# Kernel optimization log

Hardware: AMD Instinct MI355X
Metric: run time of the kernel (lower is better)

## Reference

```python
import jax, jax.numpy as jnp
import numpy as np

B, T, D, UNITS, NUM_OUT = 64, 1024, 256, 256, 32


def setup_inputs() -> dict:
    key = jax.random.key(0)
    k1, k2, k3 = jax.random.split(key, 3)
    inputs = jax.random.normal(k1, (B, T, D), dtype=jnp.float32)
    U = jax.random.normal(k2, (D, 4 * UNITS), dtype=jnp.float32) * 0.05
    W = jax.random.normal(k3, (UNITS, 4 * UNITS), dtype=jnp.float32) * 0.05
    b = jnp.zeros((4 * UNITS,), dtype=jnp.float32)
    return {"inputs": inputs, "U": U, "W": W, "b": b, "num_outputs": NUM_OUT}


def reference(inputs, U, W, b, num_outputs):
    # inputs: [B, T, D]; U: [D, 4u]; W: [u, 4u]; b: [4u]
    Bsz, Tlen, _ = inputs.shape
    units = W.shape[0]
    # Precompute input projection as one batched GEMM (x_t @ U + b for all t)
    xz = jnp.einsum('btd,dk->btk', inputs, U) + b  # [B, T, 4u]

    def step(carry, xz_t):
        h, c = carry
        z = xz_t + h @ W  # [B, 4u]
        z0, z1, z2, z3 = jnp.split(z, 4, axis=1)
        i = jax.nn.sigmoid(z0)
        f = jax.nn.sigmoid(z1)
        c_new = f * c + i * jnp.tanh(z2)
        o = jax.nn.sigmoid(z3)
        h_new = o * jnp.tanh(c_new)
        return (h_new, c_new), h_new

    h0 = jnp.zeros((Bsz, units), dtype=inputs.dtype)
    c0 = jnp.zeros((Bsz, units), dtype=inputs.dtype)
    (_, _), hs = jax.lax.scan(step, (h0, c0), jnp.swapaxes(xz, 0, 1))  # hs: [T, B, u]
    outputs = jnp.swapaxes(hs, 0, 1)[:, Tlen - num_outputs:, :]  # [B, num_outputs, u]
    return outputs
```

## Files before the change

### kernel.cpp

```cpp
#include <hip/hip_runtime.h>
#include <hip/hip_fp16.h>
#include <stdint.h>

#define Bsz 64
#define Tsz 1024
#define Dsz 256
#define UNITSn 256
#define Zdim 1024

typedef _Float16 half2v __attribute__((ext_vector_type(2)));
typedef _Float16 f16x8  __attribute__((ext_vector_type(8)));
typedef float    f32x4  __attribute__((ext_vector_type(4)));

__device__ __forceinline__ float dot2acc(uint32_t w, uint32_t h, float acc) {
#if __has_builtin(__builtin_amdgcn_fdot2)
  return __builtin_amdgcn_fdot2(__builtin_bit_cast(half2v, w),
                                __builtin_bit_cast(half2v, h), acc, false);
#else
  __half2 wv = __builtin_bit_cast(__half2, w);
  __half2 hv = __builtin_bit_cast(__half2, h);
  acc = fmaf(__half2float(__low2half(wv)),  __half2float(__low2half(hv)),  acc);
  acc = fmaf(__half2float(__high2half(wv)), __half2float(__high2half(hv)), acc);
  return acc;
#endif
}

__device__ __forceinline__ float dot4(const uint4& w, const uint4& h, float acc) {
  acc = dot2acc(w.x, h.x, acc); acc = dot2acc(w.y, h.y, acc);
  acc = dot2acc(w.z, h.z, acc); acc = dot2acc(w.w, h.w, acc);
  return acc;
}

__device__ __forceinline__ float sigm(float x)   { return 1.0f / (1.0f + __expf(-x)); }
__device__ __forceinline__ float tanh_f(float x) { return 1.0f - 2.0f / (__expf(2.0f * x) + 1.0f); }

__global__ __launch_bounds__(256) void convert_u(const float* __restrict__ U,
                                                 _Float16* __restrict__ UT) {
  int i = blockIdx.x * 256 + threadIdx.x;
  int n = i >> 8, k = i & 255;
  UT[i] = (_Float16)U[(size_t)k * Zdim + n];
}

__global__ __launch_bounds__(256) void convert_w5(const float* __restrict__ W,
                                                  uint4* __restrict__ Wop,
                                                  uint4* __restrict__ Wlds,
                                                  uint4* __restrict__ Wstr) {
  int i = blockIdx.x * 256 + threadIdx.x;
  if (i >= 32768) return;
  int t, g, k2base, outIdx;
  uint4* dst;
  if (i < 8192) {
    int j = i >> 9; t = i & 511; g = j & 3; k2base = (j >> 2) * 4;
    dst = Wop; outIdx = i;
  } else if (i < 14336) {
    int i2 = i - 8192; int cl = i2 >> 9; t = i2 & 511; g = cl & 3;
    k2base = 16 + (cl >> 2) * 4; dst = Wlds; outIdx = i2;
  } else {
    int i3 = i - 14336; int kb = i3 >> 11; int r = i3 & 2047;
    t = r >> 2; g = r & 3; k2base = 28 + kb * 4; dst = Wstr; outIdx = i3;
  }
  int col = g * 256 + (t & 255);
  int kbase = (t >> 8) * 64 + k2base;
  uint32_t d[4];
#pragma unroll
  for (int e = 0; e < 4; e++) {
    int k2 = kbase + e;
    float w0 = W[(size_t)(2 * k2) * Zdim + col];
    float w1 = W[(size_t)(2 * k2 + 1) * Zdim + col];
    __half2 p = __floats2half2_rn(w0, w1);
    d[e] = __builtin_bit_cast(uint32_t, p);
  }
  dst[outIdx] = make_uint4(d[0], d[1], d[2], d[3]);
}

__global__ __launch_bounds__(256) void proj_mfma(
    const float* __restrict__ x, const _Float16* __restrict__ UT,
    const float* __restrict__ bias, float* __restrict__ xz, int t0) {
  __shared__ _Float16 Ax[64][40];
  __shared__ _Float16 Ux[256][40];
  const int tid  = threadIdx.x;
  const int w    = tid >> 6, lane = tid & 63;
  const int lr   = lane & 15, kg = lane >> 4;
  const int n0   = blockIdx.x * 256;
  const int tloc = blockIdx.y;
  const int t    = t0 + tloc;
  const int arow = tid >> 2, ak = (tid & 3) * 8;

  f32x4 acc[4][4];
#pragma unroll
  for (int mi = 0; mi < 4; mi++)
#pragma unroll
    for (int ni = 0; ni < 4; ni++) acc[mi][ni] = f32x4{0.f, 0.f, 0.f, 0.f};

  for (int k0 = 0; k0 < Dsz; k0 += 32) {
    const float* xp = x + ((size_t)arow * Tsz + t) * Dsz + k0 + ak;
    float4 p0 = *(const float4*)xp;
    float4 p1 = *(const float4*)(xp + 4);
    const _Float16* up = UT + (size_t)(n0 + tid) * Dsz + k0;
    f16x8 u0 = *(const f16x8*)up;
    f16x8 u1 = *(const f16x8*)(up + 8);
    f16x8 u2 = *(const f16x8*)(up + 16);
    f16x8 u3 = *(const f16x8*)(up + 24);
    __syncthreads();
    f16x8 a8;
    a8[0] = (_Float16)p0.x; a8[1] = (_Float16)p0.y;
    a8[2] = (_Float16)p0.z; a8[3] = (_Float16)p0.w;
    a8[4] = (_Float16)p1.x; a8[5] = (_Float16)p1.y;
    a8[6] = (_Float16)p1.z; a8[7] = (_Float16)p1.w;
    *(f16x8*)&Ax[arow][ak] = a8;
    *(f16x8*)&Ux[tid][0]  = u0;
    *(f16x8*)&Ux[tid][8]  = u1;
    *(f16x8*)&Ux[tid][16] = u2;
    *(f16x8*)&Ux[tid][24] = u3;
    __syncthreads();
    f16x8 af[4], uf[4];
#pragma unroll
    for (int mi = 0; mi < 4; mi++) af[mi] = *(const f16x8*)&Ax[mi * 16 + lr][kg * 8];
#pragma unroll
    for (int ni = 0; ni < 4; ni++) uf[ni] = *(const f16x8*)&Ux[w * 64 + ni * 16 + lr][kg * 8];
#pragma unroll
    for (int mi = 0; mi < 4; mi++)
#pragma unroll
      for (int ni = 0; ni < 4; ni++)
        acc[mi][ni] = __builtin_amdgcn_mfma_f32_16x16x32_f16(af[mi], uf[ni],
                                                             acc[mi][ni], 0, 0, 0);
  }
#pragma unroll
  for (int ni = 0; ni < 4; ni++) {
    int col = n0 + w * 64 + ni * 16 + lr;
    float bs = bias[col];
#pragma unroll
    for (int mi = 0; mi < 4; mi++) {
      f32x4 v = acc[mi][ni];
#pragma unroll
      for (int r = 0; r < 4; r++) {
        int brow = mi * 16 + kg * 4 + r;
        xz[((size_t)tloc * 64 + brow) * Zdim + col] = v[r] + bs;
      }
    }
  }
}

__global__ __launch_bounds__(512) void lstm_chunk(
    const float* __restrict__ xz, const uint4* __restrict__ Wop,
    const uint4* __restrict__ WldsBuf, const uint4* __restrict__ Wstr,
    float* __restrict__ out, uint4* __restrict__ h_state,
    float* __restrict__ c_state, int t0, int Tc, int n_out) {
  extern __shared__ uint4 smem4[];
  uint4*  Wl = smem4;
  uint4*  hq = smem4 + 6144;
  float4* pp = (float4*)(smem4 + 6144 + 64);

  const int tid  = threadIdx.x;
  const int b    = blockIdx.x;
  const int half = tid >> 8, u = tid & 255;

  uint4 wop[16];
#pragma unroll
  for (int j = 0; j < 16; j++) wop[j] = Wop[(size_t)j * 512 + tid];
#pragma unroll
  for (int j = 0; j < 16; j++)
    asm volatile("" : "+v"(wop[j].x), "+v"(wop[j].y), "+v"(wop[j].z), "+v"(wop[j].w));
#pragma unroll
  for (int cl = 0; cl < 12; cl++)
    Wl[(size_t)cl * 512 + tid] = WldsBuf[(size_t)cl * 512 + tid];

  float c = 0.0f;
  if (t0 == 0) {
    if (tid < 64) hq[tid] = make_uint4(0, 0, 0, 0);
  } else {
    if (tid < 32) hq[tid] = h_state[(size_t)b * 32 + tid];
    if (half == 0) c = c_state[(size_t)b * 256 + u];
  }
  __syncthreads();

  const float* xzb = xz + (size_t)b * Zdim + u;
  float nx0 = 0, nx1 = 0, nx2 = 0, nx3 = 0;
  if (half == 0) { nx0 = xzb[0]; nx1 = xzb[256]; nx2 = xzb[512]; nx3 = xzb[768]; }
  const uint4* wstr = Wstr + (size_t)tid * 4;

#define LDB(s, kb) { const uint4* p_ = wstr + (size_t)(kb) * 2048; \
    s[0] = p_[0]; s[1] = p_[1]; s[2] = p_[2]; s[3] = p_[3]; }
#define USEB(s, hi) { uint4 h4_ = hb[hi]; \
    a0 = dot4(s[0], h4_, a0); a1 = dot4(s[1], h4_, a1); \
    a2 = dot4(s[2], h4_, a2); a3 = dot4(s[3], h4_, a3); }
#define LDSPH(jj2) { uint4 h4_ = hb[4 + (jj2)]; \
    uint4 w0_ = Wl[(size_t)((jj2) * 4 + 0) * 512 + tid]; \
    uint4 w1_ = Wl[(size_t)((jj2) * 4 + 1) * 512 + tid]; \
    uint4 w2_ = Wl[(size_t)((jj2) * 4 + 2) * 512 + tid]; \
    uint4 w3_ = Wl[(size_t)((jj2) * 4 + 3) * 512 + tid]; \
    a0 = dot4(w0_, h4_, a0); a1 = dot4(w1_, h4_, a1); \
    a2 = dot4(w2_, h4_, a2); a3 = dot4(w3_, h4_, a3); }

  for (int tl = 0; tl < Tc; tl++) {
    const int buf = tl & 1;
    const uint4* hb = hq + buf * 32 + half * 16;
    float a0 = 0, a1 = 0, a2 = 0, a3 = 0;
    uint4 sA[4], sB[4];
    LDB(sA, 0); LDB(sB, 1);
#pragma unroll
    for (int jj = 0; jj < 4; jj++) {
      uint4 h4 = hb[jj];
      a0 = dot4(wop[jj * 4 + 0], h4, a0);
      a1 = dot4(wop[jj * 4 + 1], h4, a1);
      a2 = dot4(wop[jj * 4 + 2], h4, a2);
      a3 = dot4(wop[jj * 4 + 3], h4, a3);
    }
    USEB(sA, 7);  LDB(sA, 2);
    LDSPH(0);
    USEB(sB, 8);  LDB(sB, 3);
    LDSPH(1);
    USEB(sA, 9);  LDB(sA, 4);
    LDSPH(2);
    USEB(sB, 10); LDB(sB, 5);
    USEB(sA, 11); LDB(sA, 6);
    USEB(sB, 12); LDB(sB, 7);
    USEB(sA, 13); LDB(sA, 8);
    USEB(sB, 14);
    USEB(sA, 15);

    if (half) pp[u] = make_float4(a0, a1, a2, a3);
    __syncthreads();
    if (!half) {
      float4 q = pp[u];
      float z0 = a0 + q.x + nx0, z1 = a1 + q.y + nx1;
      float z2 = a2 + q.z + nx2, z3 = a3 + q.w + nx3;
      if (tl + 1 < Tc) {
        const float* xn = xzb + (size_t)(tl + 1) * (Bsz * Zdim);
        nx0 = xn[0]; nx1 = xn[256]; nx2 = xn[512]; nx3 = xn[768];
      }
      float ig = sigm(z0), fg = sigm(z1), gg = tanh_f(z2), og = sigm(z3);
      c = fg * c + ig * gg;
      float hn = og * tanh_f(c);
      int ot = (t0 + tl) - (Tsz - n_out);
      if (ot >= 0) out[((size_t)b * n_out + ot) * UNITSn + u] = hn;
      ((__half*)(hq + (buf ^ 1) * 32))[u] = __float2half(hn);
    }
    __syncthreads();
  }
  if (tid < 32) h_state[(size_t)b * 32 + tid] = hq[(Tc & 1) * 32 + tid];
  if (half == 0) c_state[(size_t)b * 256 + u] = c;
#undef LDB
#undef USEB
#undef LDSPH
}

extern "C" void kernel_launch(void* const* d_in, const int* in_sizes, int n_in,
                              void* d_out, int out_size, void* d_ws, size_t ws_size,
                              hipStream_t stream) {
  const float* x    = (const float*)d_in[0];
  const float* U    = (const float*)d_in[1];
  const float* W    = (const float*)d_in[2];
  const float* bias = (const float*)d_in[3];
  float* out = (float*)d_out;
  const int n_out = out_size / (Bsz * UNITSn);

  uint8_t* ws = (uint8_t*)d_ws;
  uint4* Wop      = (uint4*)ws;
  uint4* Wlds     = (uint4*)(ws + (128u << 10));
  uint4* Wstr     = (uint4*)(ws + (224u << 10));
  _Float16* UT    = (_Float16*)(ws + (512u << 10));
  uint4* h_state  = (uint4*)(ws + (1024u << 10));
  float* c_state  = (float*)(ws + (1056u << 10));
  float* xz       = (float*)(ws + (2u << 20));

  int Tc = Tsz;
  while (Tc > 1 && (size_t)(2u << 20) + (size_t)Tc * (Bsz * Zdim) * 4 > ws_size) Tc >>= 1;

  convert_w5<<<dim3(128), dim3(256), 0, stream>>>(W, Wop, Wlds, Wstr);
  convert_u<<<dim3(1024), dim3(256), 0, stream>>>(U, UT);

  const int ldsBytes = (6144 + 64 + 256) * 16;
  hipFuncSetAttribute((const void*)lstm_chunk,
                      hipFuncAttributeMaxDynamicSharedMemorySize, ldsBytes);

  for (int t0 = 0; t0 < Tsz; t0 += Tc) {
    proj_mfma<<<dim3(4, Tc), dim3(256), 0, stream>>>(x, UT, bias, xz, t0);
    lstm_chunk<<<dim3(Bsz), dim3(512), ldsBytes, stream>>>(xz, Wop, Wlds, Wstr,
                                                           out, h_state, c_state,
                                                           t0, Tc, n_out);
  }
}
```

Before: 1.813 ms.

## Split recurrent K-dimension across four thread quarters per batch block

The recurrent LSTM kernel moves from 512 threads (two K-halves) to 1024 threads (four K-quarters) per batch row, so each thread handles 64 of the 256 hidden inputs. The weight split changes to match: 16 register slots, 8 LDS slots and 8 streamed-from-global slots per thread, with the converter rewritten for the new layout. Partial sums from three quarters go through LDS and quarter 0 reduces them, aiming to shorten the serial per-timestep dot-product chain. The dot product now uses inline v_dot2_f32_f16 asm instead of the builtin. In exchange it uses more LDS, more threads and a larger reduction per step.

```diff
diff --git a/kernel.cpp b/kernel.cpp
--- a/kernel.cpp
+++ b/kernel.cpp
@@ -8,21 +8,12 @@
 #define UNITSn 256
 #define Zdim 1024
 
-typedef _Float16 half2v __attribute__((ext_vector_type(2)));
 typedef _Float16 f16x8  __attribute__((ext_vector_type(8)));
 typedef float    f32x4  __attribute__((ext_vector_type(4)));
 
 __device__ __forceinline__ float dot2acc(uint32_t w, uint32_t h, float acc) {
-#if __has_builtin(__builtin_amdgcn_fdot2)
-  return __builtin_amdgcn_fdot2(__builtin_bit_cast(half2v, w),
-                                __builtin_bit_cast(half2v, h), acc, false);
-#else
-  __half2 wv = __builtin_bit_cast(__half2, w);
-  __half2 hv = __builtin_bit_cast(__half2, h);
-  acc = fmaf(__half2float(__low2half(wv)),  __half2float(__low2half(hv)),  acc);
-  acc = fmaf(__half2float(__high2half(wv)), __half2float(__high2half(hv)), acc);
+  asm("v_dot2_f32_f16 %0, %1, %2, %0" : "+v"(acc) : "v"(w), "v"(h));
   return acc;
-#endif
 }
 
 __device__ __forceinline__ float dot4(const uint4& w, const uint4& h, float acc) {
@@ -41,26 +32,21 @@
   UT[i] = (_Float16)U[(size_t)k * Zdim + n];
 }
 
-__global__ __launch_bounds__(256) void convert_w5(const float* __restrict__ W,
+__global__ __launch_bounds__(256) void convert_w6(const float* __restrict__ W,
                                                   uint4* __restrict__ Wop,
                                                   uint4* __restrict__ Wlds,
                                                   uint4* __restrict__ Wstr) {
   int i = blockIdx.x * 256 + threadIdx.x;
   if (i >= 32768) return;
-  int t, g, k2base, outIdx;
+  int slot = i >> 10, t = i & 1023;
+  int q = t >> 8, u = t & 255;
+  int g, j, outIdx;
   uint4* dst;
-  if (i < 8192) {
-    int j = i >> 9; t = i & 511; g = j & 3; k2base = (j >> 2) * 4;
-    dst = Wop; outIdx = i;
-  } else if (i < 14336) {
-    int i2 = i - 8192; int cl = i2 >> 9; t = i2 & 511; g = cl & 3;
-    k2base = 16 + (cl >> 2) * 4; dst = Wlds; outIdx = i2;
-  } else {
-    int i3 = i - 14336; int kb = i3 >> 11; int r = i3 & 2047;
-    t = r >> 2; g = r & 3; k2base = 28 + kb * 4; dst = Wstr; outIdx = i3;
-  }
-  int col = g * 256 + (t & 255);
-  int kbase = (t >> 8) * 64 + k2base;
+  if (slot < 16)      { g = slot >> 2;      j = slot & 3;            dst = Wop;  outIdx = slot * 1024 + t; }
+  else if (slot < 24) { int cl = slot - 16; g = cl & 3; j = 4 + (cl >> 2); dst = Wlds; outIdx = cl * 1024 + t; }
+  else                { int ss = slot - 24; g = ss & 3; j = 6 + (ss >> 2); dst = Wstr; outIdx = ss * 1024 + t; }
+  int col = g * 256 + u;
+  int kbase = q * 32 + j * 4;
   uint32_t d[4];
 #pragma unroll
   for (int e = 0; e < 4; e++) {
@@ -141,90 +127,85 @@
   }
 }
 
-__global__ __launch_bounds__(512) void lstm_chunk(
-    const float* __restrict__ xz, const uint4* __restrict__ Wop,
-    const uint4* __restrict__ WldsBuf, const uint4* __restrict__ Wstr,
-    float* __restrict__ out, uint4* __restrict__ h_state,
-    float* __restrict__ c_state, int t0, int Tc, int n_out) {
+__global__ __launch_bounds__(1024)
+__attribute__((amdgpu_waves_per_eu(4, 4)))
+void lstm_chunk(const float* __restrict__ xz, const uint4* __restrict__ Wop,
+                const uint4* __restrict__ WldsBuf, const uint4* __restrict__ Wstr,
+                float* __restrict__ out, uint4* __restrict__ h_state,
+                float* __restrict__ c_state, int t0, int Tc, int n_out) {
   extern __shared__ uint4 smem4[];
   uint4*  Wl = smem4;
-  uint4*  hq = smem4 + 6144;
-  float4* pp = (float4*)(smem4 + 6144 + 64);
-
-  const int tid  = threadIdx.x;
-  const int b    = blockIdx.x;
-  const int half = tid >> 8, u = tid & 255;
+  uint4*  hq = smem4 + 8192;
+  float4* pp = (float4*)(smem4 + 8192 + 64);
+
+  const int tid = threadIdx.x;
+  const int b   = blockIdx.x;
+  const int q   = tid >> 8, u = tid & 255;
 
   uint4 wop[16];
 #pragma unroll
-  for (int j = 0; j < 16; j++) wop[j] = Wop[(size_t)j * 512 + tid];
+  for (int j = 0; j < 16; j++) wop[j] = Wop[(size_t)j * 1024 + tid];
 #pragma unroll
   for (int j = 0; j < 16; j++)
     asm volatile("" : "+v"(wop[j].x), "+v"(wop[j].y), "+v"(wop[j].z), "+v"(wop[j].w));
 #pragma unroll
-  for (int cl = 0; cl < 12; cl++)
-    Wl[(size_t)cl * 512 + tid] = WldsBuf[(size_t)cl * 512 + tid];
+  for (int cl = 0; cl < 8; cl++)
+    Wl[(size_t)cl * 1024 + tid] = WldsBuf[(size_t)cl * 1024 + tid];
 
   float c = 0.0f;
   if (t0 == 0) {
     if (tid < 64) hq[tid] = make_uint4(0, 0, 0, 0);
   } else {
     if (tid < 32) hq[tid] = h_state[(size_t)b * 32 + tid];
-    if (half == 0) c = c_state[(size_t)b * 256 + u];
+    if (q == 0)   c = c_state[(size_t)b * 256 + u];
   }
   __syncthreads();
 
   const float* xzb = xz + (size_t)b * Zdim + u;
   float nx0 = 0, nx1 = 0, nx2 = 0, nx3 = 0;
-  if (half == 0) { nx0 = xzb[0]; nx1 = xzb[256]; nx2 = xzb[512]; nx3 = xzb[768]; }
-  const uint4* wstr = Wstr + (size_t)tid * 4;
-
-#define LDB(s, kb) { const uint4* p_ = wstr + (size_t)(kb) * 2048; \
-    s[0] = p_[0]; s[1] = p_[1]; s[2] = p_[2]; s[3] = p_[3]; }
-#define USEB(s, hi) { uint4 h4_ = hb[hi]; \
-    a0 = dot4(s[0], h4_, a0); a1 = dot4(s[1], h4_, a1); \
-    a2 = dot4(s[2], h4_, a2); a3 = dot4(s[3], h4_, a3); }
-#define LDSPH(jj2) { uint4 h4_ = hb[4 + (jj2)]; \
-    uint4 w0_ = Wl[(size_t)((jj2) * 4 + 0) * 512 + tid]; \
-    uint4 w1_ = Wl[(size_t)((jj2) * 4 + 1) * 512 + tid]; \
-    uint4 w2_ = Wl[(size_t)((jj2) * 4 + 2) * 512 + tid]; \
-    uint4 w3_ = Wl[(size_t)((jj2) * 4 + 3) * 512 + tid]; \
-    a0 = dot4(w0_, h4_, a0); a1 = dot4(w1_, h4_, a1); \
-    a2 = dot4(w2_, h4_, a2); a3 = dot4(w3_, h4_, a3); }
+  if (q == 0) { nx0 = xzb[0]; nx1 = xzb[256]; nx2 = xzb[512]; nx3 = xzb[768]; }
+  const uint4* wstr = Wstr + tid;
 
   for (int tl = 0; tl < Tc; tl++) {
     const int buf = tl & 1;
-    const uint4* hb = hq + buf * 32 + half * 16;
+    const uint4* hb = hq + buf * 32 + q * 8;
     float a0 = 0, a1 = 0, a2 = 0, a3 = 0;
-    uint4 sA[4], sB[4];
-    LDB(sA, 0); LDB(sB, 1);
-#pragma unroll
-    for (int jj = 0; jj < 4; jj++) {
-      uint4 h4 = hb[jj];
-      a0 = dot4(wop[jj * 4 + 0], h4, a0);
-      a1 = dot4(wop[jj * 4 + 1], h4, a1);
-      a2 = dot4(wop[jj * 4 + 2], h4, a2);
-      a3 = dot4(wop[jj * 4 + 3], h4, a3);
-    }
-    USEB(sA, 7);  LDB(sA, 2);
-    LDSPH(0);
-    USEB(sB, 8);  LDB(sB, 3);
-    LDSPH(1);
-    USEB(sA, 9);  LDB(sA, 4);
-    LDSPH(2);
-    USEB(sB, 10); LDB(sB, 5);
-    USEB(sA, 11); LDB(sA, 6);
-    USEB(sB, 12); LDB(sB, 7);
-    USEB(sA, 13); LDB(sA, 8);
-    USEB(sB, 14);
-    USEB(sA, 15);
-
-    if (half) pp[u] = make_float4(a0, a1, a2, a3);
-    __syncthreads();
-    if (!half) {
-      float4 q = pp[u];
-      float z0 = a0 + q.x + nx0, z1 = a1 + q.y + nx1;
-      float z2 = a2 + q.z + nx2, z3 = a3 + q.w + nx3;
+
+    uint4 sA0 = wstr[0], sA1 = wstr[1024], sA2 = wstr[2048], sA3 = wstr[3072];
+#pragma unroll
+    for (int j = 0; j < 4; j++) {
+      uint4 h4 = hb[j];
+      a0 = dot4(wop[0 * 4 + j], h4, a0);
+      a1 = dot4(wop[1 * 4 + j], h4, a1);
+      a2 = dot4(wop[2 * 4 + j], h4, a2);
+      a3 = dot4(wop[3 * 4 + j], h4, a3);
+    }
+    uint4 sB0 = wstr[4096], sB1 = wstr[5120], sB2 = wstr[6144], sB3 = wstr[7168];
+#pragma unroll
+    for (int jj = 0; jj < 2; jj++) {
+      uint4 h4 = hb[4 + jj];
+      uint4 w0 = Wl[(size_t)(jj * 4 + 0) * 1024 + tid];
+      uint4 w1 = Wl[(size_t)(jj * 4 + 1) * 1024 + tid];
+      uint4 w2 = Wl[(size_t)(jj * 4 + 2) * 1024 + tid];
+      uint4 w3 = Wl[(size_t)(jj * 4 + 3) * 1024 + tid];
+      a0 = dot4(w0, h4, a0); a1 = dot4(w1, h4, a1);
+      a2 = dot4(w2, h4, a2); a3 = dot4(w3, h4, a3);
+    }
+    { uint4 h4 = hb[6];
+      a0 = dot4(sA0, h4, a0); a1 = dot4(sA1, h4, a1);
+      a2 = dot4(sA2, h4, a2); a3 = dot4(sA3, h4, a3); }
+    { uint4 h4 = hb[7];
+      a0 = dot4(sB0, h4, a0); a1 = dot4(sB1, h4, a1);
+      a2 = dot4(sB2, h4, a2); a3 = dot4(sB3, h4, a3); }
+
+    if (q) pp[(size_t)(q - 1) * 256 + u] = make_float4(a0, a1, a2, a3);
+    __syncthreads();
+    if (!q) {
+      float4 p0 = pp[u], p1 = pp[256 + u], p2 = pp[512 + u];
+      float z0 = a0 + p0.x + p1.x + p2.x + nx0;
+      float z1 = a1 + p0.y + p1.y + p2.y + nx1;
+      float z2 = a2 + p0.z + p1.z + p2.z + nx2;
+      float z3 = a3 + p0.w + p1.w + p2.w + nx3;
       if (tl + 1 < Tc) {
         const float* xn = xzb + (size_t)(tl + 1) * (Bsz * Zdim);
         nx0 = xn[0]; nx1 = xn[256]; nx2 = xn[512]; nx3 = xn[768];
@@ -239,10 +220,7 @@
     __syncthreads();
   }
   if (tid < 32) h_state[(size_t)b * 32 + tid] = hq[(Tc & 1) * 32 + tid];
-  if (half == 0) c_state[(size_t)b * 256 + u] = c;
-#undef LDB
-#undef USEB
-#undef LDSPH
+  if (q == 0)   c_state[(size_t)b * 256 + u] = c;
 }
 
 extern "C" void kernel_launch(void* const* d_in, const int* in_sizes, int n_in,
@@ -257,8 +235,8 @@
 
   uint8_t* ws = (uint8_t*)d_ws;
   uint4* Wop      = (uint4*)ws;
-  uint4* Wlds     = (uint4*)(ws + (128u << 10));
-  uint4* Wstr     = (uint4*)(ws + (224u << 10));
+  uint4* Wlds     = (uint4*)(ws + (256u << 10));
+  uint4* Wstr     = (uint4*)(ws + (384u << 10));
   _Float16* UT    = (_Float16*)(ws + (512u << 10));
   uint4* h_state  = (uint4*)(ws + (1024u << 10));
   float* c_state  = (float*)(ws + (1056u << 10));
@@ -267,17 +245,17 @@
   int Tc = Tsz;
   while (Tc > 1 && (size_t)(2u << 20) + (size_t)Tc * (Bsz * Zdim) * 4 > ws_size) Tc >>= 1;
 
-  convert_w5<<<dim3(128), dim3(256), 0, stream>>>(W, Wop, Wlds, Wstr);
+  convert_w6<<<dim3(128), dim3(256), 0, stream>>>(W, Wop, Wlds, Wstr);
   convert_u<<<dim3(1024), dim3(256), 0, stream>>>(U, UT);
 
-  const int ldsBytes = (6144 + 64 + 256) * 16;
+  const int ldsBytes = (8192 + 64 + 768) * 16;
   hipFuncSetAttribute((const void*)lstm_chunk,
                       hipFuncAttributeMaxDynamicSharedMemorySize, ldsBytes);
 
   for (int t0 = 0; t0 < Tsz; t0 += Tc) {
     proj_mfma<<<dim3(4, Tc), dim3(256), 0, stream>>>(x, UT, bias, xz, t0);
-    lstm_chunk<<<dim3(Bsz), dim3(512), ldsBytes, stream>>>(xz, Wop, Wlds, Wstr,
-                                                           out, h_state, c_state,
-                                                           t0, Tc, n_out);
-  }
-}
+    lstm_chunk<<<dim3(Bsz), dim3(1024), ldsBytes, stream>>>(xz, Wop, Wlds, Wstr,
+                                                            out, h_state, c_state,
+                                                            t0, Tc, n_out);
+  }
+}
```

New measurement: 2.241 ms. +23.7%, slower.

## Hold more recurrent weights in registers and cut streamed global loads in LSTM step

Applied to the files above, without the earlier changes.

The split of the recurrent weight matrix W across storage tiers changes: registers now hold 40 uint4 slices per thread (up from 16), LDS keeps 12, and the part streamed from global/L2 each timestep shrinks from 9 blocks of 4 to 3 blocks of 4. The conversion kernel is rewritten to match the new layout, shared memory becomes static, and the dot product uses inline v_dot2_f32_f16 asm. The aim is to cut per-step global memory traffic on the serial recurrence critical path. The cost is much higher VGPR pressure (160 registers just for weights), which risks spills or an occupancy limit at 512 threads.

```diff
diff --git a/kernel.cpp b/kernel.cpp
--- a/kernel.cpp
+++ b/kernel.cpp
@@ -8,21 +8,12 @@
 #define UNITSn 256
 #define Zdim 1024
 
-typedef _Float16 half2v __attribute__((ext_vector_type(2)));
 typedef _Float16 f16x8  __attribute__((ext_vector_type(8)));
 typedef float    f32x4  __attribute__((ext_vector_type(4)));
 
 __device__ __forceinline__ float dot2acc(uint32_t w, uint32_t h, float acc) {
-#if __has_builtin(__builtin_amdgcn_fdot2)
-  return __builtin_amdgcn_fdot2(__builtin_bit_cast(half2v, w),
-                                __builtin_bit_cast(half2v, h), acc, false);
-#else
-  __half2 wv = __builtin_bit_cast(__half2, w);
-  __half2 hv = __builtin_bit_cast(__half2, h);
-  acc = fmaf(__half2float(__low2half(wv)),  __half2float(__low2half(hv)),  acc);
-  acc = fmaf(__half2float(__high2half(wv)), __half2float(__high2half(hv)), acc);
+  asm("v_dot2_f32_f16 %0, %1, %2, %0" : "+v"(acc) : "v"(w), "v"(h));
   return acc;
-#endif
 }
 
 __device__ __forceinline__ float dot4(const uint4& w, const uint4& h, float acc) {
@@ -41,26 +32,20 @@
   UT[i] = (_Float16)U[(size_t)k * Zdim + n];
 }
 
-__global__ __launch_bounds__(256) void convert_w5(const float* __restrict__ W,
+__global__ __launch_bounds__(256) void convert_w7(const float* __restrict__ W,
                                                   uint4* __restrict__ Wop,
                                                   uint4* __restrict__ Wlds,
                                                   uint4* __restrict__ Wstr) {
   int i = blockIdx.x * 256 + threadIdx.x;
   if (i >= 32768) return;
-  int t, g, k2base, outIdx;
+  int slot = i >> 9, t = i & 511;
+  int g, jx, outIdx;
   uint4* dst;
-  if (i < 8192) {
-    int j = i >> 9; t = i & 511; g = j & 3; k2base = (j >> 2) * 4;
-    dst = Wop; outIdx = i;
-  } else if (i < 14336) {
-    int i2 = i - 8192; int cl = i2 >> 9; t = i2 & 511; g = cl & 3;
-    k2base = 16 + (cl >> 2) * 4; dst = Wlds; outIdx = i2;
-  } else {
-    int i3 = i - 14336; int kb = i3 >> 11; int r = i3 & 2047;
-    t = r >> 2; g = r & 3; k2base = 28 + kb * 4; dst = Wstr; outIdx = i3;
-  }
+  if (slot < 40)      { g = slot / 10;      jx = slot % 10;        dst = Wop;  outIdx = slot * 512 + t; }
+  else if (slot < 52) { int ss = slot - 40; g = ss & 3; jx = 10 + (ss >> 2); dst = Wlds; outIdx = ss * 512 + t; }
+  else                { int ss = slot - 52; g = ss & 3; jx = 13 + (ss >> 2); dst = Wstr; outIdx = ss * 512 + t; }
   int col = g * 256 + (t & 255);
-  int kbase = (t >> 8) * 64 + k2base;
+  int kbase = (t >> 8) * 64 + jx * 4;
   uint32_t d[4];
 #pragma unroll
   for (int e = 0; e < 4; e++) {
@@ -146,20 +131,19 @@
     const uint4* __restrict__ WldsBuf, const uint4* __restrict__ Wstr,
     float* __restrict__ out, uint4* __restrict__ h_state,
     float* __restrict__ c_state, int t0, int Tc, int n_out) {
-  extern __shared__ uint4 smem4[];
-  uint4*  Wl = smem4;
-  uint4*  hq = smem4 + 6144;
-  float4* pp = (float4*)(smem4 + 6144 + 64);
+  __shared__ uint4 Wl[12 * 512];
+  __shared__ uint4 hq[2][32];
+  __shared__ float4 pp[256];
 
   const int tid  = threadIdx.x;
   const int b    = blockIdx.x;
   const int half = tid >> 8, u = tid & 255;
 
-  uint4 wop[16];
-#pragma unroll
-  for (int j = 0; j < 16; j++) wop[j] = Wop[(size_t)j * 512 + tid];
-#pragma unroll
-  for (int j = 0; j < 16; j++)
+  uint4 wop[40];
+#pragma unroll
+  for (int j = 0; j < 40; j++) wop[j] = Wop[(size_t)j * 512 + tid];
+#pragma unroll
+  for (int j = 0; j < 40; j++)
     asm volatile("" : "+v"(wop[j].x), "+v"(wop[j].y), "+v"(wop[j].z), "+v"(wop[j].w));
 #pragma unroll
   for (int cl = 0; cl < 12; cl++)
@@ -167,9 +151,9 @@
 
   float c = 0.0f;
   if (t0 == 0) {
-    if (tid < 64) hq[tid] = make_uint4(0, 0, 0, 0);
+    if (tid < 64) ((uint4*)hq)[tid] = make_uint4(0, 0, 0, 0);
   } else {
-    if (tid < 32) hq[tid] = h_state[(size_t)b * 32 + tid];
+    if (tid < 32) ((uint4*)hq)[tid] = h_state[(size_t)b * 32 + tid];
     if (half == 0) c = c_state[(size_t)b * 256 + u];
   }
   __syncthreads();
@@ -177,47 +161,50 @@
   const float* xzb = xz + (size_t)b * Zdim + u;
   float nx0 = 0, nx1 = 0, nx2 = 0, nx3 = 0;
   if (half == 0) { nx0 = xzb[0]; nx1 = xzb[256]; nx2 = xzb[512]; nx3 = xzb[768]; }
-  const uint4* wstr = Wstr + (size_t)tid * 4;
-
-#define LDB(s, kb) { const uint4* p_ = wstr + (size_t)(kb) * 2048; \
-    s[0] = p_[0]; s[1] = p_[1]; s[2] = p_[2]; s[3] = p_[3]; }
-#define USEB(s, hi) { uint4 h4_ = hb[hi]; \
-    a0 = dot4(s[0], h4_, a0); a1 = dot4(s[1], h4_, a1); \
-    a2 = dot4(s[2], h4_, a2); a3 = dot4(s[3], h4_, a3); }
-#define LDSPH(jj2) { uint4 h4_ = hb[4 + (jj2)]; \
-    uint4 w0_ = Wl[(size_t)((jj2) * 4 + 0) * 512 + tid]; \
-    uint4 w1_ = Wl[(size_t)((jj2) * 4 + 1) * 512 + tid]; \
-    uint4 w2_ = Wl[(size_t)((jj2) * 4 + 2) * 512 + tid]; \
-    uint4 w3_ = Wl[(size_t)((jj2) * 4 + 3) * 512 + tid]; \
-    a0 = dot4(w0_, h4_, a0); a1 = dot4(w1_, h4_, a1); \
-    a2 = dot4(w2_, h4_, a2); a3 = dot4(w3_, h4_, a3); }
+  const uint4* wstr = Wstr + tid;
 
   for (int tl = 0; tl < Tc; tl++) {
     const int buf = tl & 1;
-    const uint4* hb = hq + buf * 32 + half * 16;
+    const uint4* hb = hq[buf] + half * 16;
     float a0 = 0, a1 = 0, a2 = 0, a3 = 0;
-    uint4 sA[4], sB[4];
-    LDB(sA, 0); LDB(sB, 1);
-#pragma unroll
-    for (int jj = 0; jj < 4; jj++) {
-      uint4 h4 = hb[jj];
-      a0 = dot4(wop[jj * 4 + 0], h4, a0);
-      a1 = dot4(wop[jj * 4 + 1], h4, a1);
-      a2 = dot4(wop[jj * 4 + 2], h4, a2);
-      a3 = dot4(wop[jj * 4 + 3], h4, a3);
+
+    uint4 s00 = wstr[0 * 512], s01 = wstr[1 * 512], s02 = wstr[2 * 512], s03 = wstr[3 * 512];
+    uint4 s10 = wstr[4 * 512], s11 = wstr[5 * 512], s12 = wstr[6 * 512], s13 = wstr[7 * 512];
+
+#pragma unroll
+    for (int j = 0; j < 10; j++) {
+      uint4 h4 = hb[j];
+      a0 = dot4(wop[0 * 10 + j], h4, a0);
+      a1 = dot4(wop[1 * 10 + j], h4, a1);
+      a2 = dot4(wop[2 * 10 + j], h4, a2);
+      a3 = dot4(wop[3 * 10 + j], h4, a3);
     }
-    USEB(sA, 7);  LDB(sA, 2);
-    LDSPH(0);
-    USEB(sB, 8);  LDB(sB, 3);
-    LDSPH(1);
-    USEB(sA, 9);  LDB(sA, 4);
-    LDSPH(2);
-    USEB(sB, 10); LDB(sB, 5);
-    USEB(sA, 11); LDB(sA, 6);
-    USEB(sB, 12); LDB(sB, 7);
-    USEB(sA, 13); LDB(sA, 8);
-    USEB(sB, 14);
-    USEB(sA, 15);
+    uint4 s20, s21, s22, s23;
+    { uint4 h4 = hb[13];
+      s20 = wstr[8 * 512]; s21 = wstr[9 * 512]; s22 = wstr[10 * 512]; s23 = wstr[11 * 512];
+      a0 = dot4(s00, h4, a0); a1 = dot4(s01, h4, a1);
+      a2 = dot4(s02, h4, a2); a3 = dot4(s03, h4, a3); }
+    { uint4 h4 = hb[10];
+      uint4 w0 = Wl[(size_t)0 * 512 + tid], w1 = Wl[(size_t)1 * 512 + tid];
+      uint4 w2 = Wl[(size_t)2 * 512 + tid], w3 = Wl[(size_t)3 * 512 + tid];
+      a0 = dot4(w0, h4, a0); a1 = dot4(w1, h4, a1);
+      a2 = dot4(w2, h4, a2); a3 = dot4(w3, h4, a3); }
+    { uint4 h4 = hb[14];
+      a0 = dot4(s10, h4, a0); a1 = dot4(s11, h4, a1);
+      a2 = dot4(s12, h4, a2); a3 = dot4(s13, h4, a3); }
+    { uint4 h4 = hb[11];
+      uint4 w0 = Wl[(size_t)4 * 512 + tid], w1 = Wl[(size_t)5 * 512 + tid];
+      uint4 w2 = Wl[(size_t)6 * 512 + tid], w3 = Wl[(size_t)7 * 512 + tid];
+      a0 = dot4(w0, h4, a0); a1 = dot4(w1, h4, a1);
+      a2 = dot4(w2, h4, a2); a3 = dot4(w3, h4, a3); }
+    { uint4 h4 = hb[15];
+      a0 = dot4(s20, h4, a0); a1 = dot4(s21, h4, a1);
+      a2 = dot4(s22, h4, a2); a3 = dot4(s23, h4, a3); }
+    { uint4 h4 = hb[12];
+      uint4 w0 = Wl[(size_t)8 * 512 + tid], w1 = Wl[(size_t)9 * 512 + tid];
+      uint4 w2 = Wl[(size_t)10 * 512 + tid], w3 = Wl[(size_t)11 * 512 + tid];
+      a0 = dot4(w0, h4, a0); a1 = dot4(w1, h4, a1);
+      a2 = dot4(w2, h4, a2); a3 = dot4(w3, h4, a3); }
 
     if (half) pp[u] = make_float4(a0, a1, a2, a3);
     __syncthreads();
@@ -234,15 +221,12 @@
       float hn = og * tanh_f(c);
       int ot = (t0 + tl) - (Tsz - n_out);
       if (ot >= 0) out[((size_t)b * n_out + ot) * UNITSn + u] = hn;
-      ((__half*)(hq + (buf ^ 1) * 32))[u] = __float2half(hn);
+      ((__half*)hq[buf ^ 1])[u] = __float2half(hn);
     }
     __syncthreads();
   }
-  if (tid < 32) h_state[(size_t)b * 32 + tid] = hq[(Tc & 1) * 32 + tid];
+  if (tid < 32) h_state[(size_t)b * 32 + tid] = ((uint4*)hq)[(Tc & 1) * 32 + tid];
   if (half == 0) c_state[(size_t)b * 256 + u] = c;
-#undef LDB
-#undef USEB
-#undef LDSPH
 }
 
 extern "C" void kernel_launch(void* const* d_in, const int* in_sizes, int n_in,
@@ -257,8 +241,8 @@
 
   uint8_t* ws = (uint8_t*)d_ws;
   uint4* Wop      = (uint4*)ws;
-  uint4* Wlds     = (uint4*)(ws + (128u << 10));
-  uint4* Wstr     = (uint4*)(ws + (224u << 10));
+  uint4* Wlds     = (uint4*)(ws + (320u << 10));
+  uint4* Wstr     = (uint4*)(ws + (416u << 10));
   _Float16* UT    = (_Float16*)(ws + (512u << 10));
   uint4* h_state  = (uint4*)(ws + (1024u << 10));
   float* c_state  = (float*)(ws + (1056u << 10));
@@ -267,17 +251,13 @@
   int Tc = Tsz;
   while (Tc > 1 && (size_t)(2u << 20) + (size_t)Tc * (Bsz * Zdim) * 4 > ws_size) Tc >>= 1;
 
-  convert_w5<<<dim3(128), dim3(256), 0, stream>>>(W, Wop, Wlds, Wstr);
+  convert_w7<<<dim3(128), dim3(256), 0, stream>>>(W, Wop, Wlds, Wstr);
   convert_u<<<dim3(1024), dim3(256), 0, stream>>>(U, UT);
-
-  const int ldsBytes = (6144 + 64 + 256) * 16;
-  hipFuncSetAttribute((const void*)lstm_chunk,
-                      hipFuncAttributeMaxDynamicSharedMemorySize, ldsBytes);
 
   for (int t0 = 0; t0 < Tsz; t0 += Tc) {
     proj_mfma<<<dim3(4, Tc), dim3(256), 0, stream>>>(x, UT, bias, xz, t0);
-    lstm_chunk<<<dim3(Bsz), dim3(512), ldsBytes, stream>>>(xz, Wop, Wlds, Wstr,
-                                                           out, h_state, c_state,
-                                                           t0, Tc, n_out);
-  }
-}
+    lstm_chunk<<<dim3(Bsz), dim3(512), 0, stream>>>(xz, Wop, Wlds, Wstr,
+                                                    out, h_state, c_state,
+                                                    t0, Tc, n_out);
+  }
+}
```

After: 2.129 ms. +17.4%, slower.
